# Performance work log

Hardware: AMD Instinct MI355X
Metric: run time of the kernel (lower is better)

## Reference

```python
import jax, jax.numpy as jnp
import numpy as np

B, S, D, E, K = 4, 4096, 4096, 64, 2

def setup_inputs() -> dict:
    key = jax.random.key(0)
    kx, kw = jax.random.split(key)
    x = jax.random.normal(kx, (B, S, D), dtype=jnp.float32)
    # nn.Linear weight is [out_features, in_features] = [n_experts, d_model]
    W = jax.random.normal(kw, (E, D), dtype=jnp.float32) * (1.0 / np.sqrt(D))
    return {"x": x, "W": W, "k": K}

def reference(x, W, k):
    # logits = x @ W^T : [B, S, E]
    logits = jnp.einsum('bsd,ed->bse', x, W)
    probs = jax.nn.softmax(logits, axis=-1)
    values, indices = jax.lax.top_k(probs, k)  # [B, S, k]
    return (probs, indices, values)
```

## Files before the change

### kernel.cpp

```cpp
#include <hip/hip_runtime.h>


#define TOK 16384
#define DIM 4096
#define NE  64
#define BK  64
#define NT  (DIM / BK)
#define IDX_OFF (TOK * NE)
#define VAL_OFF (IDX_OFF + TOK * 2)

typedef __attribute__((ext_vector_type(8))) short short8;
typedef __attribute__((ext_vector_type(4))) float f32x4;
union pk8u { unsigned int u[4]; short8 s; };

__device__ __forceinline__ unsigned int pack_hi(float fa, float fb) {
    return __builtin_amdgcn_perm(__float_as_uint(fb), __float_as_uint(fa), 0x07060302u);
}
__device__ __forceinline__ unsigned int pack_lo(float fa, float fb) {
    float la = fa - __uint_as_float(__float_as_uint(fa) & 0xffff0000u);
    float lb = fb - __uint_as_float(__float_as_uint(fb) & 0xffff0000u);
    return __builtin_amdgcn_perm(__float_as_uint(lb), __float_as_uint(la), 0x07060302u);
}
__device__ __forceinline__ void split8(const float4 v0, const float4 v1,
                                       short8& hi, short8& lo) {
    pk8u h, l;
    h.u[0] = pack_hi(v0.x, v0.y); l.u[0] = pack_lo(v0.x, v0.y);
    h.u[1] = pack_hi(v0.z, v0.w); l.u[1] = pack_lo(v0.z, v0.w);
    h.u[2] = pack_hi(v1.x, v1.y); l.u[2] = pack_lo(v1.x, v1.y);
    h.u[3] = pack_hi(v1.z, v1.w); l.u[3] = pack_lo(v1.z, v1.w);
    hi = h.s; lo = l.s;
}

__global__ __launch_bounds__(256)
void wconv_kernel(const float* __restrict__ W, unsigned short* __restrict__ ws) {
    const int gid = blockIdx.x * 256 + threadIdx.x;
    const int l = gid & 63;
    const int r = gid >> 6;
    const int h = r & 1;
    const int g = (r >> 1) & 3;
    const int c = (r >> 3) & 1;
    const int t = r >> 4;
    const int e = g * 16 + (l & 15);
    const int k = t * 64 + c * 32 + (l >> 4) * 8;
    const float4 va = *(const float4*)(W + (size_t)e * DIM + k);
    const float4 vb = *(const float4*)(W + (size_t)e * DIM + k + 4);
    pk8u o;
    if (h == 0) {
        o.u[0] = pack_hi(va.x, va.y); o.u[1] = pack_hi(va.z, va.w);
        o.u[2] = pack_hi(vb.x, vb.y); o.u[3] = pack_hi(vb.z, vb.w);
    } else {
        o.u[0] = pack_lo(va.x, va.y); o.u[1] = pack_lo(va.z, va.w);
        o.u[2] = pack_lo(vb.x, vb.y); o.u[3] = pack_lo(vb.z, vb.w);
    }
    ((uint4*)ws)[gid] = *(uint4*)&o.u[0];
}

__global__ __launch_bounds__(512)
void router_mfma(const float* __restrict__ x,
                 const unsigned short* __restrict__ wsg,
                 float* __restrict__ out)
{
    __shared__ __align__(16) float          xs[3 * 4096];
    __shared__ __align__(16) unsigned short wls[3 * 8192];
    __shared__ __align__(16) float          lgt[64 * 68];

    const int tid  = threadIdx.x;
    const int lane = tid & 63;
    const int wid  = __builtin_amdgcn_readfirstlane(tid >> 6);
    const int t0   = blockIdx.x * 64;
    const int c16  = lane & 15;
    const int q    = lane >> 4;
    const int tp   = wid & 3;
    const int eh   = wid >> 2;

    auto issue = [&](int tt, int b) {
#pragma unroll
        for (int i = 0; i < 2; ++i) {
            const int u   = wid * 2 + i;
            const int p   = u * 64 + lane;
            const int tok = p >> 4;
            const int m   = (p & 15) ^ (tok & 7);
            const float* src = x + (size_t)(t0 + tok) * DIM + tt * BK + m * 4;
            __builtin_amdgcn_global_load_lds(
                (const __attribute__((address_space(1))) unsigned int*)src,
                (__attribute__((address_space(3))) unsigned int*)&xs[b * 4096 + u * 256],
                16, 0, 0);
        }
#pragma unroll
        for (int i = 0; i < 2; ++i) {
            const int v = wid * 2 + i;
            const unsigned short* src = wsg + ((size_t)(tt * 16 + v) * 64 + lane) * 8;
            __builtin_amdgcn_global_load_lds(
                (const __attribute__((address_space(1))) unsigned int*)src,
                (__attribute__((address_space(3))) unsigned int*)&wls[b * 8192 + v * 512],
                16, 0, 0);
        }
    };

    f32x4 acc0 = {0.f, 0.f, 0.f, 0.f};
    f32x4 acc1 = {0.f, 0.f, 0.f, 0.f};

    issue(0, 0);
    issue(1, 1);
    int b = 0;
    for (int t = 0; t < NT; ++t) {
        if (t < NT - 1)
            asm volatile("s_waitcnt vmcnt(4) lgkmcnt(0)\n\ts_barrier" ::: "memory");
        else
            asm volatile("s_waitcnt vmcnt(0) lgkmcnt(0)\n\ts_barrier" ::: "memory");
        if (t + 2 < NT) issue(t + 2, (b + 2) % 3);

        const float*          xb = &xs[b * 4096];
        const unsigned short* wb = &wls[b * 8192];
#pragma unroll
        for (int c = 0; c < 2; ++c) {
            const int tokA = tp * 16 + c16;
            const int m1   = c * 8 + q * 2;
            const float4 a0 = *(const float4*)(xb + (tokA * 16 + ( m1      ^ (tokA & 7))) * 4);
            const float4 a1 = *(const float4*)(xb + (tokA * 16 + ((m1 + 1) ^ (tokA & 7))) * 4);
            short8 ah, al;
            split8(a0, a1, ah, al);
#pragma unroll
            for (int g2 = 0; g2 < 2; ++g2) {
                const int g = eh * 2 + g2;
                const int vb_ = ((c * 4 + g) * 2) * 512 + lane * 8;
                const short8 bh = *(const short8*)(wb + vb_);
                const short8 bl = *(const short8*)(wb + vb_ + 512);
                f32x4& A = g2 ? acc1 : acc0;
                A = __builtin_amdgcn_mfma_f32_16x16x32_bf16(ah, bh, A, 0, 0, 0);
                A = __builtin_amdgcn_mfma_f32_16x16x32_bf16(al, bh, A, 0, 0, 0);
                A = __builtin_amdgcn_mfma_f32_16x16x32_bf16(ah, bl, A, 0, 0, 0);
            }
        }
        b = (b + 1) % 3;
    }

#pragma unroll
    for (int r = 0; r < 4; ++r) {
        lgt[(tp * 16 + q * 4 + r) * 68 + (eh * 2 + 0) * 16 + c16] = acc0[r];
        lgt[(tp * 16 + q * 4 + r) * 68 + (eh * 2 + 1) * 16 + c16] = acc1[r];
    }
    __syncthreads();

    if (tid < 64) {
        const int tkn = t0 + tid;
        float* row = lgt + tid * 68;
        float m = -3.0e38f;
#pragma unroll
        for (int e4 = 0; e4 < NE; e4 += 4) {
            const float4 v = *(const float4*)(row + e4);
            m = fmaxf(m, fmaxf(fmaxf(v.x, v.y), fmaxf(v.z, v.w)));
        }
        float sum = 0.f, v1 = -3.0e38f, v2 = -3.0e38f;
        int i1 = 0, i2 = 0;
#pragma unroll
        for (int e4 = 0; e4 < NE; e4 += 4) {
            const float4 v = *(const float4*)(row + e4);
            sum += __expf(v.x - m) + __expf(v.y - m) + __expf(v.z - m) + __expf(v.w - m);
            const float* pv = &v.x;
#pragma unroll
            for (int j = 0; j < 4; ++j) {
                const float p = pv[j];
                const int e = e4 + j;
                if (p > v1)      { v2 = v1; i2 = i1; v1 = p; i1 = e; }
                else if (p > v2) { v2 = p;  i2 = e; }
            }
        }
        const float inv = 1.f / sum;
        row[64] = m; row[65] = inv;
        out[IDX_OFF + (size_t)tkn * 2]     = (float)i1;
        out[IDX_OFF + (size_t)tkn * 2 + 1] = (float)i2;
        out[VAL_OFF + (size_t)tkn * 2]     = __expf(v1 - m) * inv;
        out[VAL_OFF + (size_t)tkn * 2 + 1] = __expf(v2 - m) * inv;
    }
    __syncthreads();

    {
        const int row = tid >> 3;
        const int e8  = (tid & 7) * 8;
        const float m   = lgt[row * 68 + 64];
        const float inv = lgt[row * 68 + 65];
        const float4 v0 = *(const float4*)(lgt + row * 68 + e8);
        const float4 v1 = *(const float4*)(lgt + row * 68 + e8 + 4);
        float4 p0, p1;
        p0.x = __expf(v0.x - m) * inv; p0.y = __expf(v0.y - m) * inv;
        p0.z = __expf(v0.z - m) * inv; p0.w = __expf(v0.w - m) * inv;
        p1.x = __expf(v1.x - m) * inv; p1.y = __expf(v1.y - m) * inv;
        p1.z = __expf(v1.z - m) * inv; p1.w = __expf(v1.w - m) * inv;
        float* dst = out + (size_t)(t0 + row) * NE + e8;
        *(float4*)dst       = p0;
        *(float4*)(dst + 4) = p1;
    }
}

__global__ __launch_bounds__(64)
void fallback_kernel(const float* __restrict__ x, const float* __restrict__ W,
                     float* __restrict__ out) {
    const int tk = blockIdx.x * 64 + threadIdx.x;
    const float* xr = x + (size_t)tk * DIM;
    float lg[NE];
    float m = -3.0e38f;
    for (int e = 0; e < NE; ++e) {
        const float* wr = W + (size_t)e * DIM;
        float s = 0.f;
        for (int d = 0; d < DIM; d += 4) {
            const float4 a = *(const float4*)(xr + d);
            const float4 bb = *(const float4*)(wr + d);
            s += a.x * bb.x + a.y * bb.y + a.z * bb.z + a.w * bb.w;
        }
        lg[e] = s; m = fmaxf(m, s);
    }
    float sum = 0.f;
    for (int e = 0; e < NE; ++e) sum += __expf(lg[e] - m);
    const float inv = 1.f / sum;
    float v1 = -3.0e38f, v2 = -3.0e38f; int i1 = 0, i2 = 0;
    for (int e = 0; e < NE; ++e) {
        const float p = __expf(lg[e] - m) * inv;
        out[(size_t)tk * NE + e] = p;
        if (p > v1)      { v2 = v1; i2 = i1; v1 = p; i1 = e; }
        else if (p > v2) { v2 = p;  i2 = e; }
    }
    out[IDX_OFF + (size_t)tk * 2]     = (float)i1;
    out[IDX_OFF + (size_t)tk * 2 + 1] = (float)i2;
    out[VAL_OFF + (size_t)tk * 2]     = v1;
    out[VAL_OFF + (size_t)tk * 2 + 1] = v2;
}

extern "C" void kernel_launch(void* const* d_in, const int* in_sizes, int n_in,
                              void* d_out, int out_size, void* d_ws, size_t ws_size,
                              hipStream_t stream) {
    const float* x = (const float*)d_in[0];
    const float* W = (const float*)d_in[1];
    float* out = (float*)d_out;
    (void)in_sizes; (void)n_in; (void)out_size;

    if (ws_size >= (size_t)NE * DIM * 2 * 2) {
        wconv_kernel<<<256, 256, 0, stream>>>(W, (unsigned short*)d_ws);
        router_mfma<<<TOK / 64, 512, 0, stream>>>(x, (const unsigned short*)d_ws, out);
    } else {
        fallback_kernel<<<TOK / 64, 64, 0, stream>>>(x, W, out);
    }
}
```

Before: 423.0 us.

## Replace LDS triple-buffered staging with direct register double-buffered global loads

Drops the shared-memory staging of x and bf16 weight tiles, whose async global_load_lds copies were synchronised by a barrier on every k-step. Each wave now loads its own x and weight fragments straight from global memory into registers, double-buffered across two tiles, so the main loop needs no barriers. Blocks shrink to 32 tokens and 256 threads with a 3-blocks-per-CU hint, giving more blocks and less shared memory per block. In exchange, weight fragments are re-read from global/L2 by every wave with no LDS reuse, register pressure rises, and x loads are strided per lane rather than swizzled.

```diff
diff --git a/kernel.cpp b/kernel.cpp
--- a/kernel.cpp
+++ b/kernel.cpp
@@ -55,84 +55,77 @@
     ((uint4*)ws)[gid] = *(uint4*)&o.u[0];
 }
 
-__global__ __launch_bounds__(512)
+struct TR {
+    float4 x0, x1, x2, x3;
+    short8 w0, w1, w2, w3, w4, w5, w6, w7;
+};
+
+__device__ __forceinline__ void load_tile(TR& r, const float* bx,
+                                          const unsigned short* bw, int t) {
+    const float* px = bx + t * BK;
+    r.x0 = *(const float4*)(px);
+    r.x1 = *(const float4*)(px + 4);
+    r.x2 = *(const float4*)(px + 32);
+    r.x3 = *(const float4*)(px + 36);
+    const unsigned short* pw = bw + (size_t)t * 8192;
+    r.w0 = *(const short8*)(pw);
+    r.w1 = *(const short8*)(pw + 512);
+    r.w2 = *(const short8*)(pw + 1024);
+    r.w3 = *(const short8*)(pw + 1536);
+    r.w4 = *(const short8*)(pw + 4096);
+    r.w5 = *(const short8*)(pw + 4608);
+    r.w6 = *(const short8*)(pw + 5120);
+    r.w7 = *(const short8*)(pw + 5632);
+}
+
+__device__ __forceinline__ void compute_tile(const TR& r, f32x4& acc0, f32x4& acc1) {
+    short8 ah, al;
+    split8(r.x0, r.x1, ah, al);
+    acc0 = __builtin_amdgcn_mfma_f32_16x16x32_bf16(ah, r.w0, acc0, 0, 0, 0);
+    acc0 = __builtin_amdgcn_mfma_f32_16x16x32_bf16(al, r.w0, acc0, 0, 0, 0);
+    acc0 = __builtin_amdgcn_mfma_f32_16x16x32_bf16(ah, r.w1, acc0, 0, 0, 0);
+    acc1 = __builtin_amdgcn_mfma_f32_16x16x32_bf16(ah, r.w2, acc1, 0, 0, 0);
+    acc1 = __builtin_amdgcn_mfma_f32_16x16x32_bf16(al, r.w2, acc1, 0, 0, 0);
+    acc1 = __builtin_amdgcn_mfma_f32_16x16x32_bf16(ah, r.w3, acc1, 0, 0, 0);
+    split8(r.x2, r.x3, ah, al);
+    acc0 = __builtin_amdgcn_mfma_f32_16x16x32_bf16(ah, r.w4, acc0, 0, 0, 0);
+    acc0 = __builtin_amdgcn_mfma_f32_16x16x32_bf16(al, r.w4, acc0, 0, 0, 0);
+    acc0 = __builtin_amdgcn_mfma_f32_16x16x32_bf16(ah, r.w5, acc0, 0, 0, 0);
+    acc1 = __builtin_amdgcn_mfma_f32_16x16x32_bf16(ah, r.w6, acc1, 0, 0, 0);
+    acc1 = __builtin_amdgcn_mfma_f32_16x16x32_bf16(al, r.w6, acc1, 0, 0, 0);
+    acc1 = __builtin_amdgcn_mfma_f32_16x16x32_bf16(ah, r.w7, acc1, 0, 0, 0);
+}
+
+__global__ __launch_bounds__(256, 3)
 void router_mfma(const float* __restrict__ x,
                  const unsigned short* __restrict__ wsg,
                  float* __restrict__ out)
 {
-    __shared__ __align__(16) float          xs[3 * 4096];
-    __shared__ __align__(16) unsigned short wls[3 * 8192];
-    __shared__ __align__(16) float          lgt[64 * 68];
+    __shared__ __align__(16) float lgt[32 * 68];
 
     const int tid  = threadIdx.x;
     const int lane = tid & 63;
-    const int wid  = __builtin_amdgcn_readfirstlane(tid >> 6);
-    const int t0   = blockIdx.x * 64;
+    const int wid  = tid >> 6;
+    const int t0   = blockIdx.x * 32;
     const int c16  = lane & 15;
     const int q    = lane >> 4;
-    const int tp   = wid & 3;
-    const int eh   = wid >> 2;
-
-    auto issue = [&](int tt, int b) {
-#pragma unroll
-        for (int i = 0; i < 2; ++i) {
-            const int u   = wid * 2 + i;
-            const int p   = u * 64 + lane;
-            const int tok = p >> 4;
-            const int m   = (p & 15) ^ (tok & 7);
-            const float* src = x + (size_t)(t0 + tok) * DIM + tt * BK + m * 4;
-            __builtin_amdgcn_global_load_lds(
-                (const __attribute__((address_space(1))) unsigned int*)src,
-                (__attribute__((address_space(3))) unsigned int*)&xs[b * 4096 + u * 256],
-                16, 0, 0);
-        }
-#pragma unroll
-        for (int i = 0; i < 2; ++i) {
-            const int v = wid * 2 + i;
-            const unsigned short* src = wsg + ((size_t)(tt * 16 + v) * 64 + lane) * 8;
-            __builtin_amdgcn_global_load_lds(
-                (const __attribute__((address_space(1))) unsigned int*)src,
-                (__attribute__((address_space(3))) unsigned int*)&wls[b * 8192 + v * 512],
-                16, 0, 0);
-        }
-    };
+    const int tp   = wid & 1;
+    const int eh   = wid >> 1;
+
+    const float* bx = x + (size_t)(t0 + tp * 16 + c16) * DIM + q * 8;
+    const unsigned short* bw = wsg + eh * 2048 + lane * 8;
 
     f32x4 acc0 = {0.f, 0.f, 0.f, 0.f};
     f32x4 acc1 = {0.f, 0.f, 0.f, 0.f};
 
-    issue(0, 0);
-    issue(1, 1);
-    int b = 0;
-    for (int t = 0; t < NT; ++t) {
-        if (t < NT - 1)
-            asm volatile("s_waitcnt vmcnt(4) lgkmcnt(0)\n\ts_barrier" ::: "memory");
-        else
-            asm volatile("s_waitcnt vmcnt(0) lgkmcnt(0)\n\ts_barrier" ::: "memory");
-        if (t + 2 < NT) issue(t + 2, (b + 2) % 3);
-
-        const float*          xb = &xs[b * 4096];
-        const unsigned short* wb = &wls[b * 8192];
-#pragma unroll
-        for (int c = 0; c < 2; ++c) {
-            const int tokA = tp * 16 + c16;
-            const int m1   = c * 8 + q * 2;
-            const float4 a0 = *(const float4*)(xb + (tokA * 16 + ( m1      ^ (tokA & 7))) * 4);
-            const float4 a1 = *(const float4*)(xb + (tokA * 16 + ((m1 + 1) ^ (tokA & 7))) * 4);
-            short8 ah, al;
-            split8(a0, a1, ah, al);
-#pragma unroll
-            for (int g2 = 0; g2 < 2; ++g2) {
-                const int g = eh * 2 + g2;
-                const int vb_ = ((c * 4 + g) * 2) * 512 + lane * 8;
-                const short8 bh = *(const short8*)(wb + vb_);
-                const short8 bl = *(const short8*)(wb + vb_ + 512);
-                f32x4& A = g2 ? acc1 : acc0;
-                A = __builtin_amdgcn_mfma_f32_16x16x32_bf16(ah, bh, A, 0, 0, 0);
-                A = __builtin_amdgcn_mfma_f32_16x16x32_bf16(al, bh, A, 0, 0, 0);
-                A = __builtin_amdgcn_mfma_f32_16x16x32_bf16(ah, bl, A, 0, 0, 0);
-            }
-        }
-        b = (b + 1) % 3;
+    TR A, B;
+    load_tile(A, bx, bw, 0);
+    load_tile(B, bx, bw, 1);
+    for (int t = 0; t < NT; t += 2) {
+        compute_tile(A, acc0, acc1);
+        if (t + 2 < NT) load_tile(A, bx, bw, t + 2);
+        compute_tile(B, acc0, acc1);
+        if (t + 3 < NT) load_tile(B, bx, bw, t + 3);
     }
 
 #pragma unroll
@@ -142,7 +135,7 @@
     }
     __syncthreads();
 
-    if (tid < 64) {
+    if (tid < 32) {
         const int tkn = t0 + tid;
         float* row = lgt + tid * 68;
         float m = -3.0e38f;
@@ -236,7 +229,7 @@
 
     if (ws_size >= (size_t)NE * DIM * 2 * 2) {
         wconv_kernel<<<256, 256, 0, stream>>>(W, (unsigned short*)d_ws);
-        router_mfma<<<TOK / 64, 512, 0, stream>>>(x, (const unsigned short*)d_ws, out);
+        router_mfma<<<TOK / 32, 256, 0, stream>>>(x, (const unsigned short*)d_ws, out);
     } else {
         fallback_kernel<<<TOK / 64, 64, 0, stream>>>(x, W, out);
     }
```

Measured after the change: 407.4 us. 3.7% less time.
